# Performance work log

Hardware: AMD Instinct MI355X
Metric: run time of the kernel (lower is better)

The kernel has to match this reference:

```python
import jax, jax.numpy as jnp
import numpy as np

DIM = 1024
HEADS = 16
HEAD_DIM = DIM // HEADS
EPS = 1e-5


def _layer_norm(z, g, b):
    m = jnp.mean(z, axis=-1, keepdims=True)
    v = jnp.var(z, axis=-1, keepdims=True)
    return (z - m) * jax.lax.rsqrt(v + EPS) * g + b


def setup_inputs() -> dict:
    key = jax.random.key(0)
    ks = jax.random.split(key, 8)
    B, T, S = 2, 2048, 2048
    x = jax.random.normal(ks[0], (B, T, DIM), dtype=jnp.float32)
    context = jax.random.normal(ks[1], (B, S, DIM), dtype=jnp.float32)
    w_qkv = jax.random.normal(ks[2], (DIM, 3 * DIM), dtype=jnp.float32) * 0.02
    b_qkv = jnp.zeros((3 * DIM,), dtype=jnp.float32)
    w_out = jax.random.normal(ks[3], (DIM, DIM), dtype=jnp.float32) * 0.02
    b_out = jnp.zeros((DIM,), dtype=jnp.float32)
    ln_g = jnp.ones((DIM,), dtype=jnp.float32)
    ln_b = jnp.zeros((DIM,), dtype=jnp.float32)
    return {"x": x, "context": context, "w_qkv": w_qkv, "b_qkv": b_qkv,
            "w_out": w_out, "b_out": b_out, "ln_g": ln_g, "ln_b": ln_b}


def reference(x, context, w_qkv, b_qkv, w_out, b_out, ln_g, ln_b):
    B, T, C = x.shape
    S = context.shape[1]
    scale = HEAD_DIM ** -0.5

    def split_heads(z):  # [B, L, C] -> [B, H, L, Dh]
        return z.reshape(z.shape[0], z.shape[1], HEADS, HEAD_DIM).transpose(0, 2, 1, 3)

    # self qkv
    qkv = _layer_norm(x, ln_g, ln_b) @ w_qkv + b_qkv  # [B, T, 3C]
    q = split_heads(qkv[..., :C])
    k = split_heads(qkv[..., C:2 * C])
    v = split_heads(qkv[..., 2 * C:])

    # context k, v from the shared qkv projection (K/V slices)
    ckv = _layer_norm(context, ln_g, ln_b) @ w_qkv + b_qkv  # [B, S, 3C]
    ck = split_heads(ckv[..., C:2 * C])
    cv = split_heads(ckv[..., 2 * C:])

    k = jnp.concatenate([k, ck], axis=2)  # [B, H, T+S, Dh]
    v = jnp.concatenate([v, cv], axis=2)

    attn = jax.nn.softmax(jnp.einsum('bhtd,bhsd->bhts', q, k) * scale, axis=-1)
    out = jnp.einsum('bhts,bhsd->bhtd', attn, v)  # [B, H, T, Dh]
    out = out.transpose(0, 2, 1, 3).reshape(B, T, C)
    return out @ w_out + b_out + x
```

## Files before the change

kernel.cpp:

```cpp
#include <hip/hip_runtime.h>
#include <stdint.h>

#define H 16
#define DH 64
#define T 2048
#define SS 2048
#define L 4096
#define DIM 1024
#define BB 2

typedef __bf16 bf16x8 __attribute__((ext_vector_type(8)));
typedef float f32x4 __attribute__((ext_vector_type(4)));
typedef float f32x16 __attribute__((ext_vector_type(16)));
typedef unsigned u32x4 __attribute__((ext_vector_type(4)));

__device__ __forceinline__ unsigned short f2bf(float f){
  unsigned u = __builtin_bit_cast(unsigned, f);
  u += 0x7fff + ((u >> 16) & 1);
  return (unsigned short)(u >> 16);
}

__device__ __forceinline__ unsigned cvt_pk_bf16(float lo, float hi){
  unsigned r;
  asm("v_cvt_pk_bf16_f32 %0, %1, %2" : "=v"(r) : "v"(lo), "v"(hi));
  return r;
}

__device__ __forceinline__ float fmax3(float a, float b, float c){
  float r;
  asm("v_max3_f32 %0, %1, %2, %3" : "=v"(r) : "v"(a), "v"(b), "v"(c));
  return r;
}

__device__ __forceinline__ void gload_lds16(const void* g, void* l){
  void* gnc = const_cast<void*>(g);
  __builtin_amdgcn_global_load_lds((__attribute__((address_space(1))) void*)gnc,
                                   (__attribute__((address_space(3))) void*)l, 16, 0, 0);
}

__global__ __launch_bounds__(256) void ln_kernel(const float* __restrict__ x, const float* __restrict__ ctx,
                          const float* __restrict__ g, const float* __restrict__ b,
                          unsigned short* __restrict__ out){
  int row = blockIdx.x;
  int tid = threadIdx.x;
  const float* src = (row < BB*T) ? (x + (size_t)row*DIM) : (ctx + (size_t)(row - BB*T)*DIM);
  float4 v = reinterpret_cast<const float4*>(src)[tid];
  float s  = v.x + v.y + v.z + v.w;
  float s2 = v.x*v.x + v.y*v.y + v.z*v.z + v.w*v.w;
  #pragma unroll
  for (int off = 32; off > 0; off >>= 1){
    s  += __shfl_down(s,  off, 64);
    s2 += __shfl_down(s2, off, 64);
  }
  __shared__ float red[8];
  if ((tid & 63) == 0){ red[(tid>>6)*2] = s; red[(tid>>6)*2+1] = s2; }
  __syncthreads();
  s  = red[0] + red[2] + red[4] + red[6];
  s2 = red[1] + red[3] + red[5] + red[7];
  float mean = s * (1.0f/DIM);
  float var  = s2 * (1.0f/DIM) - mean*mean;
  float rstd = rsqrtf(var + 1e-5f);
  float4 gg = reinterpret_cast<const float4*>(g)[tid];
  float4 bv = reinterpret_cast<const float4*>(b)[tid];
  ushort4 o;
  o.x = f2bf((v.x-mean)*rstd*gg.x + bv.x);
  o.y = f2bf((v.y-mean)*rstd*gg.y + bv.y);
  o.z = f2bf((v.z-mean)*rstd*gg.z + bv.z);
  o.w = f2bf((v.w-mean)*rstd*gg.w + bv.w);
  reinterpret_cast<ushort4*>(out + (size_t)row*DIM)[tid] = o;
}

__global__ __launch_bounds__(256) void transpose_f32_bf16(const float* __restrict__ in,
                          unsigned short* __restrict__ out, int R, int C){
  __shared__ float tile[32][33];
  int c0 = blockIdx.x*32, r0 = blockIdx.y*32;
  int tx = threadIdx.x & 31, ty = threadIdx.x >> 5;
  #pragma unroll
  for (int k = 0; k < 4; k++)
    tile[ty + k*8][tx] = in[(size_t)(r0 + ty + k*8)*C + c0 + tx];
  __syncthreads();
  #pragma unroll
  for (int k = 0; k < 4; k++)
    out[(size_t)(c0 + ty + k*8)*R + r0 + tx] = f2bf(tile[tx][ty + k*8]);
}

__global__ __launch_bounds__(256, 5) void qkv_gemm(const unsigned short* __restrict__ A,
      const unsigned short* __restrict__ Bt, const float* __restrict__ bias,
      unsigned short* __restrict__ qbuf, unsigned short* __restrict__ kbuf,
      unsigned short* __restrict__ vtbuf){
  int g = blockIdx.x;
  int xcd = g & 7, a = g >> 3;
  int w = (a < 32) ? ((a >> 2)*8 + (a & 3)) : (a + 32);
  int mblk = ((w & 7) << 3) + xcd;
  int nblk = w >> 3;
  int n0 = nblk*128, m0 = mblk*128;
  __shared__ union {
    struct { unsigned short at[2][128*32]; unsigned short bt[2][128*32]; } s;
    unsigned short ct[64][136];
    unsigned short vt[128][72];
  } u;
  int tid = threadIdx.x, lane = tid & 63, wv = tid >> 6;
  int wm = (wv >> 1)*64, wn = (wv & 1)*64;
  f32x4 acc[4][4];
  #pragma unroll
  for (int i = 0; i < 4; i++)
    #pragma unroll
    for (int j = 0; j < 4; j++) acc[i][j] = (f32x4){0.f,0.f,0.f,0.f};

  #define QSTAGE(bufi, k0) { \
    _Pragma("unroll") \
    for (int c = 0; c < 2; c++){ \
      int idx = c*256 + tid; \
      int row = idx >> 2, koff = (idx & 3)*16; \
      gload_lds16((const char*)A  + ((size_t)(m0+row)*DIM + (k0))*2 + koff, \
                  (char*)u.s.at[bufi] + (c*256 + wv*64)*16); \
      gload_lds16((const char*)Bt + ((size_t)(n0+row)*DIM + (k0))*2 + koff, \
                  (char*)u.s.bt[bufi] + (c*256 + wv*64)*16); \
    } }

  QSTAGE(0, 0);
  __syncthreads();

  for (int kt = 0; kt < 32; kt++){
    int bufi = kt & 1;
    if (kt + 1 < 32) QSTAGE(bufi^1, (kt+1)*32);
    bf16x8 af[4], bfv[4];
    #pragma unroll
    for (int i = 0; i < 4; i++){
      af[i]  = *reinterpret_cast<const bf16x8*>((const char*)u.s.at[bufi] + (wm + i*16 + (lane&15))*64 + (lane>>4)*16);
      bfv[i] = *reinterpret_cast<const bf16x8*>((const char*)u.s.bt[bufi] + (wn + i*16 + (lane&15))*64 + (lane>>4)*16);
    }
    #pragma unroll
    for (int mi = 0; mi < 4; mi++)
      #pragma unroll
      for (int ni = 0; ni < 4; ni++)
        acc[mi][ni] = __builtin_amdgcn_mfma_f32_16x16x32_bf16(af[mi], bfv[ni], acc[mi][ni], 0,0,0);
    __syncthreads();
  }

  int sec = n0 >> 10;
  if (sec < 2){
    float scale = (sec == 0) ? 0.18033688f : 1.0f;
    #pragma unroll
    for (int p = 0; p < 2; p++){
      __syncthreads();
      if ((wv >> 1) == p){
        #pragma unroll
        for (int ni = 0; ni < 4; ni++){
          int nl = wn + ni*16 + (lane & 15);
          float bv = bias[n0 + nl];
          #pragma unroll
          for (int mi = 0; mi < 4; mi++){
            int mloc = mi*16 + ((lane >> 4) << 2);
            #pragma unroll
            for (int r = 0; r < 4; r++)
              u.ct[mloc + r][nl] = f2bf((acc[mi][ni][r] + bv)*scale);
          }
        }
      }
      __syncthreads();
      #pragma unroll
      for (int c = 0; c < 4; c++){
        int idx = c*256 + tid;
        int row = idx >> 4, ch = idx & 15;
        bf16x8 v = *reinterpret_cast<const bf16x8*>(&u.ct[row][ch*8]);
        int gm = m0 + p*64 + row, gn = n0 + ch*8;
        int cc = gn & 1023, hh2 = cc >> 6, d = cc & 63;
        bool isctx = gm >= BB*T;
        int rm = isctx ? gm - BB*T : gm;
        int bidx = rm >> 11, tt = rm & 2047;
        size_t bh2 = (size_t)bidx*H + hh2;
        if (sec == 0){
          *reinterpret_cast<bf16x8*>(qbuf + (bh2*T + tt)*DH + d) = v;
        } else {
          int j = isctx ? T + tt : tt;
          *reinterpret_cast<bf16x8*>(kbuf + (bh2*L + j)*DH + d) = v;
        }
      }
    }
  } else {
    #pragma unroll
    for (int p = 0; p < 2; p++){
      __syncthreads();
      if ((wv >> 1) == p){
        #pragma unroll
        for (int ni = 0; ni < 4; ni++){
          int nl = wn + ni*16 + (lane & 15);
          float bv = bias[n0 + nl];
          #pragma unroll
          for (int mi = 0; mi < 4; mi++){
            int mloc = mi*16 + ((lane >> 4) << 2);
            ushort4 o;
            o.x = f2bf(acc[mi][ni][0] + bv);
            o.y = f2bf(acc[mi][ni][1] + bv);
            o.z = f2bf(acc[mi][ni][2] + bv);
            o.w = f2bf(acc[mi][ni][3] + bv);
            *reinterpret_cast<ushort4*>(&u.vt[nl][mloc]) = o;
          }
        }
      }
      __syncthreads();
      #pragma unroll
      for (int c = 0; c < 4; c++){
        int idx = c*256 + tid;
        int nl = idx >> 3, ch = idx & 7;
        bf16x8 v = *reinterpret_cast<const bf16x8*>(&u.vt[nl][ch*8]);
        int gn = n0 + nl;
        int cc = gn & 1023, hh2 = cc >> 6, d = cc & 63;
        int gm = m0 + p*64 + ch*8;
        bool isctx = gm >= BB*T;
        int rm = isctx ? gm - BB*T : gm;
        int bidx = rm >> 11, tt = rm & 2047;
        int j = isctx ? T + tt : tt;
        size_t bh2 = (size_t)bidx*H + hh2;
        *reinterpret_cast<bf16x8*>(vtbuf + (bh2*DH + d)*L + j) = v;
      }
    }
  }
}

__global__ __launch_bounds__(256, 4) void attn_kernel(const unsigned short* __restrict__ q,
      const unsigned short* __restrict__ kbuf, const unsigned short* __restrict__ vtbuf,
      unsigned short* __restrict__ obuf, float* __restrict__ mbuf, float* __restrict__ lbuf){
  int hw = blockIdx.x;
  int wid = (hw & 7)*128 + (hw >> 3);
  int qt = wid & 15, bh = (wid >> 4) & 31, cb = wid >> 9;
  int hh = bh & 15, b = bh >> 4;
  int tid = threadIdx.x, lane = tid & 63, wv = tid >> 6;
  int hi = lane >> 5, q32 = lane & 31;
  __shared__ unsigned short kt[2][64*64];
  __shared__ unsigned short vtt[2][64*64];
  size_t bhs = (size_t)b*H + hh;
  int qbase = qt*128 + wv*32;

  const unsigned short* qp = q + (bhs*T + qbase + q32)*DH + hi*8;
  bf16x8 qf[4];
  #pragma unroll
  for (int ks = 0; ks < 4; ks++)
    qf[ks] = *reinterpret_cast<const bf16x8*>(qp + ks*16);

  bf16x8 ones;
  #pragma unroll
  for (int j = 0; j < 8; j++) ones[j] = (__bf16)1.0f;

  f32x16 o_acc[2], l_vec;
  #pragma unroll
  for (int d = 0; d < 2; d++)
    #pragma unroll
    for (int i = 0; i < 16; i++) o_acc[d][i] = 0.f;
  #pragma unroll
  for (int i = 0; i < 16; i++) l_vec[i] = 0.f;
  float m_l = -1e30f;

  const char* kg = (const char*)(kbuf + bhs*(size_t)L*DH) + (size_t)cb*2048*128;
  const char* vg = (const char*)(vtbuf + bhs*(size_t)DH*L) + (size_t)cb*4096;

  #define STAGE(bufi, jt) { \
    _Pragma("unroll") \
    for (int c = 0; c < 2; c++){ \
      int idx = c*256 + tid; \
      int row = idx >> 3, c16 = idx & 7; \
      int sc16 = c16 ^ (row & 7); \
      gload_lds16(kg + (size_t)((jt)*64 + row)*128 + sc16*16, \
                  (char*)kt[bufi] + (c*256 + wv*64)*16); \
      gload_lds16(vg + (size_t)row*(L*2) + (jt)*128 + sc16*16, \
                  (char*)vtt[bufi] + (c*256 + wv*64)*16); \
    } }

  STAGE(0, 0);
  __syncthreads();

  for (int jt = 0; jt < 32; ++jt){
    int bufi = jt & 1;
    if (jt + 1 < 32) STAGE(bufi^1, jt+1);
    const char* kb = (const char*)kt[bufi];
    const char* vb = (const char*)vtt[bufi];

    f32x16 sc[2];
    #pragma unroll
    for (int t = 0; t < 2; t++)
      #pragma unroll
      for (int i = 0; i < 16; i++) sc[t][i] = 0.f;
    #pragma unroll
    for (int ks = 0; ks < 4; ks++){
      #pragma unroll
      for (int t = 0; t < 2; t++){
        int row = t*32 + q32;
        bf16x8 kf = *reinterpret_cast<const bf16x8*>(kb + row*128 + (((ks*2+hi) ^ (row&7))*16));
        sc[t] = __builtin_amdgcn_mfma_f32_32x32x16_bf16(kf, qf[ks], sc[t], 0,0,0);
      }
    }

    float rt[2];
    #pragma unroll
    for (int t = 0; t < 2; t++){
      float v0 = fmax3(sc[t][0],  sc[t][1],  sc[t][2]);
      float v1 = fmax3(sc[t][3],  sc[t][4],  sc[t][5]);
      float v2 = fmax3(sc[t][6],  sc[t][7],  sc[t][8]);
      float v3 = fmax3(sc[t][9],  sc[t][10], sc[t][11]);
      float v4 = fmax3(sc[t][12], sc[t][13], sc[t][14]);
      rt[t] = fmaxf(fmax3(v0, v1, v2), fmax3(v3, v4, sc[t][15]));
    }
    float tm = fmaxf(rt[0], rt[1]);

    if (!__all(tm - m_l <= 8.0f)){
      float tmf = fmaxf(tm, __shfl_xor(tm, 32, 64));
      float mn = fmaxf(m_l, tmf);
      float alpha = __builtin_amdgcn_exp2f(m_l - mn);
      m_l = mn;
      #pragma unroll
      for (int d = 0; d < 2; d++)
        #pragma unroll
        for (int i = 0; i < 16; i++) o_acc[d][i] *= alpha;
      l_vec[0] *= alpha;
    }
    #pragma unroll
    for (int t = 0; t < 2; t++)
      #pragma unroll
      for (int i = 0; i < 16; i++)
        sc[t][i] = __builtin_amdgcn_exp2f(sc[t][i] - m_l);

    bf16x8 pfrag[4];
    #pragma unroll
    for (int t = 0; t < 2; t++){
      #pragma unroll
      for (int half = 0; half < 2; half++){
        unsigned p01 = cvt_pk_bf16(sc[t][half*8+0], sc[t][half*8+1]);
        unsigned p23 = cvt_pk_bf16(sc[t][half*8+2], sc[t][half*8+3]);
        unsigned p45 = cvt_pk_bf16(sc[t][half*8+4], sc[t][half*8+5]);
        unsigned p67 = cvt_pk_bf16(sc[t][half*8+6], sc[t][half*8+7]);
        asm("v_permlane32_swap_b32 %0, %1" : "+v"(p01), "+v"(p45));
        asm("v_permlane32_swap_b32 %0, %1" : "+v"(p23), "+v"(p67));
        u32x4 w = (u32x4){p01, p23, p45, p67};
        pfrag[t*2 + half] = __builtin_bit_cast(bf16x8, w);
      }
    }

    #pragma unroll
    for (int ks = 0; ks < 4; ks++){
      #pragma unroll
      for (int d = 0; d < 2; d++){
        int row = d*32 + q32;
        bf16x8 vf = *reinterpret_cast<const bf16x8*>(vb + row*128 + (((ks*2+hi) ^ (row&7))*16));
        o_acc[d] = __builtin_amdgcn_mfma_f32_32x32x16_bf16(vf, pfrag[ks], o_acc[d], 0,0,0);
      }
      l_vec = __builtin_amdgcn_mfma_f32_32x32x16_bf16(ones, pfrag[ks], l_vec, 0,0,0);
    }
    __syncthreads();
  }

  float inv = 1.0f / l_vec[0];
  unsigned short* aop = obuf + (size_t)cb*BB*H*T*DH + ((size_t)bh*T + qbase + q32)*DH;
  #pragma unroll
  for (int d = 0; d < 2; d++)
    #pragma unroll
    for (int rg = 0; rg < 4; rg++){
      int d0 = d*32 + rg*8 + hi*4;
      ushort4 o;
      o.x = __builtin_bit_cast(unsigned short, (__bf16)(o_acc[d][rg*4+0]*inv));
      o.y = __builtin_bit_cast(unsigned short, (__bf16)(o_acc[d][rg*4+1]*inv));
      o.z = __builtin_bit_cast(unsigned short, (__bf16)(o_acc[d][rg*4+2]*inv));
      o.w = __builtin_bit_cast(unsigned short, (__bf16)(o_acc[d][rg*4+3]*inv));
      *reinterpret_cast<ushort4*>(aop + d0) = o;
    }
  if (hi == 0){
    size_t mi = ((size_t)cb*BB*H + bh)*T + qbase + q32;
    mbuf[mi] = m_l;
    lbuf[mi] = l_vec[0];
  }
}

__global__ __launch_bounds__(256) void attn_combine(const unsigned short* __restrict__ obuf,
      const float* __restrict__ mbuf, const float* __restrict__ lbuf,
      unsigned short* __restrict__ ao){
  int gid = blockIdx.x*256 + threadIdx.x;
  int d8 = gid & 7;
  int qg = gid >> 3;
  int qq = qg & (T-1);
  int bh = qg >> 11;
  int b = bh >> 4, h = bh & 15;
  float m0 = mbuf[(size_t)qg];
  float m1 = mbuf[(size_t)BB*H*T + qg];
  float l0 = lbuf[(size_t)qg];
  float l1 = lbuf[(size_t)BB*H*T + qg];
  float mm = fmaxf(m0, m1);
  float w0 = l0 * __builtin_amdgcn_exp2f(m0 - mm);
  float w1 = l1 * __builtin_amdgcn_exp2f(m1 - mm);
  float inv = 1.0f / (w0 + w1);
  w0 *= inv; w1 *= inv;
  bf16x8 o0 = *reinterpret_cast<const bf16x8*>(obuf + (size_t)qg*DH + d8*8);
  bf16x8 o1 = *reinterpret_cast<const bf16x8*>(obuf + (size_t)BB*H*T*DH + (size_t)qg*DH + d8*8);
  bf16x8 res;
  #pragma unroll
  for (int j = 0; j < 8; j++)
    res[j] = (__bf16)(w0*(float)o0[j] + w1*(float)o1[j]);
  *reinterpret_cast<bf16x8*>(ao + ((size_t)b*T + qq)*DIM + h*DH + d8*8) = res;
}

__global__ __launch_bounds__(256) void out_gemm(const unsigned short* __restrict__ A,
      const unsigned short* __restrict__ Bt, const float* __restrict__ bout,
      const float* __restrict__ xres, float* __restrict__ out){
  int n0 = blockIdx.x*128, m0 = blockIdx.y*64;
  __shared__ unsigned short at[2][64*32];
  __shared__ unsigned short btile[2][128*32];
  int tid = threadIdx.x, lane = tid & 63, wv = tid >> 6;
  int wm = (wv >> 1)*32, wn = (wv & 1)*64;
  f32x4 acc[2][4];
  #pragma unroll
  for (int i = 0; i < 2; i++)
    #pragma unroll
    for (int j = 0; j < 4; j++) acc[i][j] = (f32x4){0.f,0.f,0.f,0.f};

  #define OSTAGE(bufi, k0) { \
    { int row = tid >> 2, koff = (tid & 3)*16; \
      gload_lds16((const char*)A + ((size_t)(m0+row)*DIM + (k0))*2 + koff, \
                  (char*)at[bufi] + (wv*64)*16); } \
    _Pragma("unroll") \
    for (int c = 0; c < 2; c++){ \
      int idx = c*256 + tid; \
      int row = idx >> 2, koff = (idx & 3)*16; \
      gload_lds16((const char*)Bt + ((size_t)(n0+row)*DIM + (k0))*2 + koff, \
                  (char*)btile[bufi] + (c*256 + wv*64)*16); \
    } }

  OSTAGE(0, 0);
  __syncthreads();

  for (int kt = 0; kt < 32; kt++){
    int bufi = kt & 1;
    if (kt + 1 < 32) OSTAGE(bufi^1, (kt+1)*32);
    bf16x8 af[2], bfv[4];
    #pragma unroll
    for (int i = 0; i < 2; i++)
      af[i]  = *reinterpret_cast<const bf16x8*>((const char*)at[bufi] + (wm + i*16 + (lane&15))*64 + (lane>>4)*16);
    #pragma unroll
    for (int i = 0; i < 4; i++)
      bfv[i] = *reinterpret_cast<const bf16x8*>((const char*)btile[bufi] + (wn + i*16 + (lane&15))*64 + (lane>>4)*16);
    #pragma unroll
    for (int mi = 0; mi < 2; mi++)
      #pragma unroll
      for (int ni = 0; ni < 4; ni++)
        acc[mi][ni] = __builtin_amdgcn_mfma_f32_16x16x32_bf16(af[mi], bfv[ni], acc[mi][ni], 0,0,0);
    __syncthreads();
  }

  #pragma unroll
  for (int ni = 0; ni < 4; ni++){
    int gn = n0 + wn + ni*16 + (lane & 15);
    float bv = bout[gn];
    #pragma unroll
    for (int mi = 0; mi < 2; mi++){
      int gmb = m0 + wm + mi*16 + ((lane >> 4) << 2);
      #pragma unroll
      for (int r = 0; r < 4; r++){
        int gm = gmb + r;
        out[(size_t)gm*DIM + gn] = acc[mi][ni][r] + bv + xres[(size_t)gm*DIM + gn];
      }
    }
  }
}

extern "C" void kernel_launch(void* const* d_in, const int* in_sizes, int n_in,
                              void* d_out, int out_size, void* d_ws, size_t ws_size,
                              hipStream_t stream){
  const float* x    = (const float*)d_in[0];
  const float* ctx  = (const float*)d_in[1];
  const float* wqkv = (const float*)d_in[2];
  const float* bqkv = (const float*)d_in[3];
  const float* wout = (const float*)d_in[4];
  const float* bout = (const float*)d_in[5];
  const float* lng  = (const float*)d_in[6];
  const float* lnb  = (const float*)d_in[7];
  float* out = (float*)d_out;

  char* ws = (char*)d_ws;
  unsigned short* wqkvT  = (unsigned short*)ws; ws += (size_t)3072*1024*2;
  unsigned short* woutT  = (unsigned short*)ws; ws += (size_t)1024*1024*2;
  unsigned short* ln_all = (unsigned short*)ws; ws += (size_t)8192*1024*2;
  unsigned short* qbuf   = (unsigned short*)ws; ws += (size_t)BB*H*T*DH*2;
  unsigned short* kbuf   = (unsigned short*)ws; ws += (size_t)BB*H*L*DH*2;
  unsigned short* vtbuf  = (unsigned short*)ws; ws += (size_t)BB*H*DH*L*2;
  unsigned short* aobuf  = (unsigned short*)ws; ws += (size_t)BB*T*DIM*2;

  unsigned short* obuf = ln_all;
  float* mbuf = (float*)wqkvT;
  float* lbuf = mbuf + (size_t)2*BB*H*T;

  transpose_f32_bf16<<<dim3(3072/32, 1024/32), dim3(256), 0, stream>>>(wqkv, wqkvT, 1024, 3072);
  transpose_f32_bf16<<<dim3(1024/32, 1024/32), dim3(256), 0, stream>>>(wout, woutT, 1024, 1024);
  ln_kernel<<<dim3(8192), dim3(256), 0, stream>>>(x, ctx, lng, lnb, ln_all);
  qkv_gemm<<<dim3(1280), dim3(256), 0, stream>>>(ln_all, wqkvT, bqkv, qbuf, kbuf, vtbuf);
  attn_kernel<<<dim3(1024), dim3(256), 0, stream>>>(qbuf, kbuf, vtbuf, obuf, mbuf, lbuf);
  attn_combine<<<dim3(BB*H*T*8/256), dim3(256), 0, stream>>>(obuf, mbuf, lbuf, aobuf);
  out_gemm<<<dim3(1024/128, 4096/64), dim3(256), 0, stream>>>(aobuf, woutT, bout, x, out);
}
```

Measured before the change: 211.7 us.

## Restructure QKV GEMM to 256x256 tiles with 8 waves and swizzled LDS

The QKV projection GEMM moves from 128x128 tiles with 4 waves to 256x256 tiles with 8 waves, using K-steps of 64 and an XOR-swizzled LDS layout to avoid bank conflicts. Global-to-LDS prefetch of the next K slice is interleaved with the quarter-tile MFMA phases, and s_setprio raises wave priority around the MFMA bursts. The block-to-tile mapping is redone for XCD locality, skipping Q columns for context rows. The larger tiles raise arithmetic intensity and cut redundant loads, at the cost of more registers, larger LDS use, and fewer blocks (320) to balance across CUs.

```diff
diff --git a/kernel.cpp b/kernel.cpp
--- a/kernel.cpp
+++ b/kernel.cpp
@@ -84,59 +84,86 @@
     out[(size_t)(c0 + ty + k*8)*R + r0 + tx] = f2bf(tile[tx][ty + k*8]);
 }
 
-__global__ __launch_bounds__(256, 5) void qkv_gemm(const unsigned short* __restrict__ A,
+__global__ __launch_bounds__(512, 2) void qkv_gemm(const unsigned short* __restrict__ A,
       const unsigned short* __restrict__ Bt, const float* __restrict__ bias,
       unsigned short* __restrict__ qbuf, unsigned short* __restrict__ kbuf,
       unsigned short* __restrict__ vtbuf){
   int g = blockIdx.x;
-  int xcd = g & 7, a = g >> 3;
-  int w = (a < 32) ? ((a >> 2)*8 + (a & 3)) : (a + 32);
-  int mblk = ((w & 7) << 3) + xcd;
-  int nblk = w >> 3;
-  int n0 = nblk*128, m0 = mblk*128;
+  int a_ = (g >> 3) + 40*(g & 7);
+  int m_, n_;
+  if (a_ < 64){ n_ = a_ >> 4; m_ = a_ & 15; }
+  else        { int a2 = a_ - 64; n_ = 4 + (a2 >> 5); m_ = a2 & 31; }
+  int n0 = n_*256, m0 = m_*256;
   __shared__ union {
-    struct { unsigned short at[2][128*32]; unsigned short bt[2][128*32]; } s;
-    unsigned short ct[64][136];
-    unsigned short vt[128][72];
+    struct { unsigned short a[2][2][128*64]; unsigned short b[2][2][128*64]; } s;
+    unsigned short ct[128][264];
+    unsigned short vt[256][136];
   } u;
   int tid = threadIdx.x, lane = tid & 63, wv = tid >> 6;
-  int wm = (wv >> 1)*64, wn = (wv & 1)*64;
-  f32x4 acc[4][4];
-  #pragma unroll
-  for (int i = 0; i < 4; i++)
+  int l15 = lane & 15, g4 = lane >> 4;
+  int wr = wv >> 2, wc = wv & 3;
+
+  f32x4 acc[8][4];
+  #pragma unroll
+  for (int i = 0; i < 8; i++)
     #pragma unroll
     for (int j = 0; j < 4; j++) acc[i][j] = (f32x4){0.f,0.f,0.f,0.f};
 
-  #define QSTAGE(bufi, k0) { \
+  #define QS_HT(dd, isB, half, jt) { \
+    const unsigned short* _s = (isB) ? Bt : A; \
+    int _b0 = ((isB) ? n0 : m0) + (half)*128; \
+    unsigned short* _d = (isB) ? &u.s.b[dd][half][0] : &u.s.a[dd][half][0]; \
     _Pragma("unroll") \
-    for (int c = 0; c < 2; c++){ \
-      int idx = c*256 + tid; \
-      int row = idx >> 2, koff = (idx & 3)*16; \
-      gload_lds16((const char*)A  + ((size_t)(m0+row)*DIM + (k0))*2 + koff, \
-                  (char*)u.s.at[bufi] + (c*256 + wv*64)*16); \
-      gload_lds16((const char*)Bt + ((size_t)(n0+row)*DIM + (k0))*2 + koff, \
-                  (char*)u.s.bt[bufi] + (c*256 + wv*64)*16); \
+    for (int _j = 0; _j < 2; _j++){ \
+      int _i = _j*512 + tid, _r = _i >> 3, _c = (_i & 7) ^ (_r & 7); \
+      gload_lds16((const char*)_s + ((size_t)(_b0 + _r)*DIM + (jt)*64)*2 + _c*16, \
+                  (char*)_d + (_j*512 + wv*64)*16); \
     } }
 
-  QSTAGE(0, 0);
+  QS_HT(0,0,0,0); QS_HT(0,0,1,0); QS_HT(0,1,0,0); QS_HT(0,1,1,0);
   __syncthreads();
 
-  for (int kt = 0; kt < 32; kt++){
-    int bufi = kt & 1;
-    if (kt + 1 < 32) QSTAGE(bufi^1, (kt+1)*32);
-    bf16x8 af[4], bfv[4];
-    #pragma unroll
-    for (int i = 0; i < 4; i++){
-      af[i]  = *reinterpret_cast<const bf16x8*>((const char*)u.s.at[bufi] + (wm + i*16 + (lane&15))*64 + (lane>>4)*16);
-      bfv[i] = *reinterpret_cast<const bf16x8*>((const char*)u.s.bt[bufi] + (wn + i*16 + (lane&15))*64 + (lane>>4)*16);
-    }
-    #pragma unroll
-    for (int mi = 0; mi < 4; mi++)
-      #pragma unroll
-      for (int ni = 0; ni < 4; ni++)
-        acc[mi][ni] = __builtin_amdgcn_mfma_f32_16x16x32_bf16(af[mi], bfv[ni], acc[mi][ni], 0,0,0);
-    __syncthreads();
-  }
+  for (int jt = 0; jt < 16; ++jt){
+    int d = jt & 1;
+    const char* ab = (const char*)&u.s.a[d][0][0];
+    const char* bb = (const char*)&u.s.b[d][0][0];
+    #pragma unroll
+    for (int q = 0; q < 4; q++){
+      int mq = (q >> 1)*4, nq = (q & 1)*2;
+      bf16x8 af[4][2], bfr[2][2];
+      #pragma unroll
+      for (int i2 = 0; i2 < 4; i2++){
+        int ar = wr*128 + (mq + i2)*16 + l15;
+        #pragma unroll
+        for (int kk = 0; kk < 2; kk++)
+          af[i2][kk] = *reinterpret_cast<const bf16x8*>(ab + (size_t)ar*128 + (((kk*4 + g4) ^ (ar & 7))*16));
+      }
+      #pragma unroll
+      for (int nj = 0; nj < 2; nj++){
+        int bc = wc*64 + (nq + nj)*16 + l15;
+        #pragma unroll
+        for (int kk = 0; kk < 2; kk++)
+          bfr[nj][kk] = *reinterpret_cast<const bf16x8*>(bb + (size_t)bc*128 + (((kk*4 + g4) ^ (bc & 7))*16));
+      }
+      if (jt < 15){
+        if (q == 0){ QS_HT(d^1, 0, 0, jt+1); QS_HT(d^1, 0, 1, jt+1); }
+        if (q == 1){ QS_HT(d^1, 1, 0, jt+1); QS_HT(d^1, 1, 1, jt+1); }
+      }
+      __builtin_amdgcn_s_barrier();
+      __builtin_amdgcn_s_setprio(1);
+      #pragma unroll
+      for (int kk = 0; kk < 2; kk++)
+        #pragma unroll
+        for (int i2 = 0; i2 < 4; i2++)
+          #pragma unroll
+          for (int nj = 0; nj < 2; nj++)
+            acc[mq+i2][nq+nj] = __builtin_amdgcn_mfma_f32_16x16x32_bf16(af[i2][kk], bfr[nj][kk], acc[mq+i2][nq+nj], 0,0,0);
+      __builtin_amdgcn_s_setprio(0);
+      if (q == 3) asm volatile("s_waitcnt vmcnt(0)" ::: "memory");
+      __builtin_amdgcn_s_barrier();
+    }
+  }
+  __syncthreads();
 
   int sec = n0 >> 10;
   if (sec < 2){
@@ -144,14 +171,14 @@
     #pragma unroll
     for (int p = 0; p < 2; p++){
       __syncthreads();
-      if ((wv >> 1) == p){
+      if (wr == p){
         #pragma unroll
         for (int ni = 0; ni < 4; ni++){
-          int nl = wn + ni*16 + (lane & 15);
+          int nl = wc*64 + ni*16 + l15;
           float bv = bias[n0 + nl];
           #pragma unroll
-          for (int mi = 0; mi < 4; mi++){
-            int mloc = mi*16 + ((lane >> 4) << 2);
+          for (int mi = 0; mi < 8; mi++){
+            int mloc = mi*16 + (g4 << 2);
             #pragma unroll
             for (int r = 0; r < 4; r++)
               u.ct[mloc + r][nl] = f2bf((acc[mi][ni][r] + bv)*scale);
@@ -160,21 +187,21 @@
       }
       __syncthreads();
       #pragma unroll
-      for (int c = 0; c < 4; c++){
-        int idx = c*256 + tid;
-        int row = idx >> 4, ch = idx & 15;
+      for (int c = 0; c < 8; c++){
+        int idx = c*512 + tid;
+        int row = idx >> 5, ch = idx & 31;
         bf16x8 v = *reinterpret_cast<const bf16x8*>(&u.ct[row][ch*8]);
-        int gm = m0 + p*64 + row, gn = n0 + ch*8;
-        int cc = gn & 1023, hh2 = cc >> 6, d = cc & 63;
+        int gm = m0 + p*128 + row, gn = n0 + ch*8;
+        int cc = gn & 1023, hh2 = cc >> 6, dd = cc & 63;
         bool isctx = gm >= BB*T;
         int rm = isctx ? gm - BB*T : gm;
         int bidx = rm >> 11, tt = rm & 2047;
         size_t bh2 = (size_t)bidx*H + hh2;
         if (sec == 0){
-          *reinterpret_cast<bf16x8*>(qbuf + (bh2*T + tt)*DH + d) = v;
+          *reinterpret_cast<bf16x8*>(qbuf + (bh2*T + tt)*DH + dd) = v;
         } else {
           int j = isctx ? T + tt : tt;
-          *reinterpret_cast<bf16x8*>(kbuf + (bh2*L + j)*DH + d) = v;
+          *reinterpret_cast<bf16x8*>(kbuf + (bh2*L + j)*DH + dd) = v;
         }
       }
     }
@@ -182,14 +209,14 @@
     #pragma unroll
     for (int p = 0; p < 2; p++){
       __syncthreads();
-      if ((wv >> 1) == p){
+      if (wr == p){
         #pragma unroll
         for (int ni = 0; ni < 4; ni++){
-          int nl = wn + ni*16 + (lane & 15);
+          int nl = wc*64 + ni*16 + l15;
           float bv = bias[n0 + nl];
           #pragma unroll
-          for (int mi = 0; mi < 4; mi++){
-            int mloc = mi*16 + ((lane >> 4) << 2);
+          for (int mi = 0; mi < 8; mi++){
+            int mloc = mi*16 + (g4 << 2);
             ushort4 o;
             o.x = f2bf(acc[mi][ni][0] + bv);
             o.y = f2bf(acc[mi][ni][1] + bv);
@@ -201,19 +228,19 @@
       }
       __syncthreads();
       #pragma unroll
-      for (int c = 0; c < 4; c++){
-        int idx = c*256 + tid;
-        int nl = idx >> 3, ch = idx & 7;
+      for (int c = 0; c < 8; c++){
+        int idx = c*512 + tid;
+        int nl = idx >> 4, ch = idx & 15;
         bf16x8 v = *reinterpret_cast<const bf16x8*>(&u.vt[nl][ch*8]);
         int gn = n0 + nl;
-        int cc = gn & 1023, hh2 = cc >> 6, d = cc & 63;
-        int gm = m0 + p*64 + ch*8;
+        int cc = gn & 1023, hh2 = cc >> 6, dd = cc & 63;
+        int gm = m0 + p*128 + ch*8;
         bool isctx = gm >= BB*T;
         int rm = isctx ? gm - BB*T : gm;
         int bidx = rm >> 11, tt = rm & 2047;
         int j = isctx ? T + tt : tt;
         size_t bh2 = (size_t)bidx*H + hh2;
-        *reinterpret_cast<bf16x8*>(vtbuf + (bh2*DH + d)*L + j) = v;
+        *reinterpret_cast<bf16x8*>(vtbuf + (bh2*DH + dd)*L + j) = v;
       }
     }
   }
@@ -489,7 +516,7 @@
   transpose_f32_bf16<<<dim3(3072/32, 1024/32), dim3(256), 0, stream>>>(wqkv, wqkvT, 1024, 3072);
   transpose_f32_bf16<<<dim3(1024/32, 1024/32), dim3(256), 0, stream>>>(wout, woutT, 1024, 1024);
   ln_kernel<<<dim3(8192), dim3(256), 0, stream>>>(x, ctx, lng, lnb, ln_all);
-  qkv_gemm<<<dim3(1280), dim3(256), 0, stream>>>(ln_all, wqkvT, bqkv, qbuf, kbuf, vtbuf);
+  qkv_gemm<<<dim3(320), dim3(512), 0, stream>>>(ln_all, wqkvT, bqkv, qbuf, kbuf, vtbuf);
   attn_kernel<<<dim3(1024), dim3(256), 0, stream>>>(qbuf, kbuf, vtbuf, obuf, mbuf, lbuf);
   attn_combine<<<dim3(BB*H*T*8/256), dim3(256), 0, stream>>>(obuf, mbuf, lbuf, aobuf);
   out_gemm<<<dim3(1024/128, 4096/64), dim3(256), 0, stream>>>(aobuf, woutT, bout, x, out);
```

Measured after the change: 220.4 us. 1.04x slower.
